# Kernel tuning notes

Hardware: AMD Instinct MI355X
Metric: run time of the kernel (lower is better)

Reference implementation:

```python
import jax, jax.numpy as jnp
import numpy as np
from functools import partial

H = 512
V = 32000


def setup_inputs() -> dict:
    key = jax.random.key(0)
    ks = jax.random.split(key, 16)
    B, Td, Te = 16, 64, 64
    s = 0.02
    inp = {
        'input_seqs': jax.random.normal(ks[0], (B, Td, H), jnp.float32),
        'input_lengths': jax.random.randint(ks[1], (B,), 1, Td + 1, jnp.int32),
        'encoder_outputs': jax.random.normal(ks[2], (B, Te, H), jnp.float32),
        'encoder_length': jax.random.randint(ks[3], (B,), 1, Te + 1, jnp.int32),
        # GRU (1 layer, batch_first): PyTorch layout W_ih (3H,H), W_hh (3H,H)
        'W_ih': jax.random.normal(ks[4], (3 * H, H), jnp.float32) * s,
        'W_hh': jax.random.normal(ks[5], (3 * H, H), jnp.float32) * s,
        'b_ih': jnp.zeros((3 * H,), jnp.float32),
        'b_hh': jnp.zeros((3 * H,), jnp.float32),
        # Attn: W: Linear(2H -> H), v: Linear(H -> 1)
        'W_attn': jax.random.normal(ks[6], (H, 2 * H), jnp.float32) * s,
        'b_attn': jnp.zeros((H,), jnp.float32),
        'v_w': jax.random.normal(ks[7], (H,), jnp.float32) * s,
        'v_b': jnp.zeros((), jnp.float32),
        # dense: Linear(2H -> H), output: Linear(H -> V)
        'W_dense': jax.random.normal(ks[8], (H, 2 * H), jnp.float32) * s,
        'b_dense': jnp.zeros((H,), jnp.float32),
        'W_out': jax.random.normal(ks[9], (V, H), jnp.float32) * s,
        'b_out': jnp.zeros((V,), jnp.float32),
    }
    return inp


def gru_forward(x, lengths, W_ih, W_hh, b_ih, b_hh):
    # Emulates pack_padded_sequence + GRU + pad_packed_sequence:
    # hidden state frozen past each sequence's length, outputs zero there.
    B, T, Hd = x.shape
    x_proj = jnp.einsum('bth,gh->btg', x, W_ih) + b_ih  # (B,T,3H)

    def step(h, inp):
        xp, t = inp  # xp: (B,3H)
        hp = h @ W_hh.T + b_hh
        xr, xz, xn = jnp.split(xp, 3, axis=-1)
        hr, hz, hn = jnp.split(hp, 3, axis=-1)
        r = jax.nn.sigmoid(xr + hr)
        z = jax.nn.sigmoid(xz + hz)
        n = jnp.tanh(xn + r * hn)
        h_new = (1.0 - z) * n + z * h
        valid = (t < lengths)[:, None]
        h_keep = jnp.where(valid, h_new, h)
        y = jnp.where(valid, h_new, 0.0)
        return h_keep, y

    h0 = jnp.zeros((B, Hd), x.dtype)
    h_last, ys = jax.lax.scan(step, h0, (x_proj.swapaxes(0, 1), jnp.arange(T)))
    return ys.swapaxes(0, 1), h_last  # (B,T,H), (B,H)


def attn_forward(enc, dec, enc_len, dec_len, W_attn, b_attn, v_w, v_b):
    B, Te, Hd = enc.shape
    Td = dec.shape[1]
    e_mask = (jnp.arange(Te) < enc_len[:, None])  # (B,Te)
    d_mask = (jnp.arange(Td) < dec_len[:, None])  # (B,Td)
    mask = (d_mask[:, :, None] & e_mask[:, None, :]).astype(enc.dtype)  # (B,Td,Te)
    # split W on the concat axis: cat(enc,dec) @ W.T = enc@We.T + dec@Wd.T
    We, Wd = W_attn[:, :Hd], W_attn[:, Hd:]
    enc_p = jnp.einsum('beh,gh->beg', enc, We)  # (B,Te,H)
    dec_p = jnp.einsum('bdh,gh->bdg', dec, Wd)  # (B,Td,H)
    m4 = mask[..., None]
    # masked-then-projected, matching enc_outputs*mask / dec_outputs*mask in torch
    score = jnp.tanh(enc_p[:, None, :, :] * m4 + dec_p[:, :, None, :] * m4 + b_attn)  # (B,Td,Te,H)
    energy = jnp.einsum('bdeh,h->bde', score, v_w) + v_b  # (B,Td,Te)
    a = jax.nn.softmax(energy, axis=2)  # softmax over ALL Te incl. masked (faithful)
    a_m = a * mask
    s = a_m.sum(axis=2)
    s = jnp.where(s == 0, 1.0, s)
    attention = a_m / s[:, :, None]  # (B,Td,Te)
    # attention is already zero where mask==0, so enc*mask == plain enc here
    context = jnp.einsum('bde,beh->bdh', attention, enc)
    return context  # dropout is identity at eval


def reference(input_seqs, input_lengths, encoder_outputs, encoder_length,
              W_ih, W_hh, b_ih, b_hh, W_attn, b_attn, v_w, v_b,
              W_dense, b_dense, W_out, b_out):
    dec_out, h_last = gru_forward(input_seqs, input_lengths, W_ih, W_hh, b_ih, b_hh)
    context = attn_forward(encoder_outputs, dec_out, encoder_length, input_lengths,
                           W_attn, b_attn, v_w, v_b)
    outputs = jnp.concatenate((dec_out, context), axis=2)  # (B,Td,2H)
    dense = jnp.tanh(jnp.einsum('bdg,hg->bdh', outputs, W_dense) + b_dense)
    logits = jnp.einsum('bdh,vh->bdv', dense, W_out) + b_out  # (B,Td,V)
    return logits, h_last[None]  # hidden: (n_layers=1, B, H)
```

## Files before the change

kernel.cpp:

```cpp
#include <hip/hip_runtime.h>
#include <stdint.h>


#define Hdim 512
#define Vdim 32000
#define Bdim 16
#define Tdim 64
#define BT   1024
#define GANG_BLOCKS 16

typedef __attribute__((ext_vector_type(8))) short bf16x8;
typedef __attribute__((ext_vector_type(4))) float f32x4;

static __device__ __forceinline__ unsigned short f2bf(float f) {
    unsigned u = __float_as_uint(f);
    u = u + 0x7FFFu + ((u >> 16) & 1u);
    return (unsigned short)(u >> 16);
}
static __device__ __forceinline__ float bf2f(unsigned short h) {
    return __uint_as_float((unsigned)h << 16);
}
static __device__ __forceinline__ float fast_tanh(float x) {
    return 2.f / (1.f + __expf(-2.f * x)) - 1.f;
}


#define U_ZERO 8320
#define U_INP  131072
#define U_WIH  196608
#define U_WAT  131072
#define U_WDE  131072
#define U_ENC  131072
#define U_SPLIT (U_INP + U_WIH + U_WAT + U_WDE + U_ENC)
#define U_WOUT 4096000
#define U_TOT  (U_ZERO + U_SPLIT + U_WOUT)

__global__ __launch_bounds__(256) void preproc_kernel(
    const float* __restrict__ input_seqs,
    const float* __restrict__ W_ih,
    const float* __restrict__ W_attn,
    const float* __restrict__ W_dense,
    const float* __restrict__ enc,
    const float* __restrict__ W_out,
    float* __restrict__ zero_base,
    unsigned short* __restrict__ inp_h, unsigned short* __restrict__ inp_l,
    unsigned short* __restrict__ Wih_h, unsigned short* __restrict__ Wih_l,
    unsigned short* __restrict__ Wat_h, unsigned short* __restrict__ Wat_l,
    unsigned short* __restrict__ Wde_h, unsigned short* __restrict__ Wde_l,
    unsigned short* __restrict__ enc_h, unsigned short* __restrict__ enc_l,
    unsigned short* __restrict__ Wout_bf)
{
    int u = blockIdx.x * 256 + threadIdx.x;
    const int stride = gridDim.x * 256;
    for (; u < U_TOT; u += stride) {
        int r = u;
        if (r < U_ZERO) {
            float4 z; z.x = 0.f; z.y = 0.f; z.z = 0.f; z.w = 0.f;
            *(float4*)(zero_base + r * 4) = z;
            continue;
        }
        r -= U_ZERO;
        if (r >= U_SPLIT) {
            int i = (r - U_SPLIT) * 4;
            float4 v = *(const float4*)(W_out + i);
            unsigned short h[4] = {f2bf(v.x), f2bf(v.y), f2bf(v.z), f2bf(v.w)};
            *(uint2*)(Wout_bf + i) = *(const uint2*)h;
            continue;
        }
        const float* src; unsigned short* hi; unsigned short* lo;
        if (r < U_INP) { src = input_seqs; hi = inp_h; lo = inp_l; }
        else { r -= U_INP;
            if (r < U_WIH) { src = W_ih; hi = Wih_h; lo = Wih_l; }
            else { r -= U_WIH;
                if (r < U_WAT) { src = W_attn; hi = Wat_h; lo = Wat_l; }
                else { r -= U_WAT;
                    if (r < U_WDE) { src = W_dense; hi = Wde_h; lo = Wde_l; }
                    else { r -= U_WDE; src = enc; hi = enc_h; lo = enc_l; }
                }
            }
        }
        int i = r * 4;
        float4 v = *(const float4*)(src + i);
        float f[4] = {v.x, v.y, v.z, v.w};
        unsigned short h[4], l[4];
#pragma unroll
        for (int k = 0; k < 4; ++k) {
            h[k] = f2bf(f[k]);
            l[k] = f2bf(f[k] - bf2f(h[k]));
        }
        *(uint2*)(hi + i) = *(const uint2*)h;
        *(uint2*)(lo + i) = *(const uint2*)l;
    }
}


__global__ __launch_bounds__(256) void gemm_split(
    const unsigned short* __restrict__ Ah, const unsigned short* __restrict__ Al, int lda,
    const unsigned short* __restrict__ Bh, const unsigned short* __restrict__ Bl, int ldb,
    const float* __restrict__ bias,
    float* __restrict__ C, unsigned short* __restrict__ Cb, int ldc,
    int K, int act)
{
    __shared__ unsigned short AsH[128 * 40];
    __shared__ unsigned short AsL[128 * 40];
    __shared__ unsigned short BsH[128 * 40];
    __shared__ unsigned short BsL[128 * 40];
    const int tid = threadIdx.x;
    const int m0 = blockIdx.y * 128, n0 = blockIdx.x * 128;
    const int wave = tid >> 6, lane = tid & 63;
    const int wm = (wave >> 1) * 64, wn = (wave & 1) * 64;
    const int lrow = lane & 15, lk = (lane >> 4) * 8;

    f32x4 acc[4][4];
#pragma unroll
    for (int i = 0; i < 4; ++i)
#pragma unroll
        for (int j = 0; j < 4; ++j) acc[i][j] = (f32x4){0.f, 0.f, 0.f, 0.f};

    for (int k0 = 0; k0 < K; k0 += 32) {
#pragma unroll
        for (int i = 0; i < 2; ++i) {
            int idx = tid + i * 256;
            int rr = idx >> 2, kq = (idx & 3) * 8;
            size_t ao = (size_t)(m0 + rr) * lda + k0 + kq;
            size_t bo = (size_t)(n0 + rr) * ldb + k0 + kq;
            *(uint4*)(&AsH[rr * 40 + kq]) = *(const uint4*)(Ah + ao);
            *(uint4*)(&AsL[rr * 40 + kq]) = *(const uint4*)(Al + ao);
            *(uint4*)(&BsH[rr * 40 + kq]) = *(const uint4*)(Bh + bo);
            *(uint4*)(&BsL[rr * 40 + kq]) = *(const uint4*)(Bl + bo);
        }
        __syncthreads();
        bf16x8 ah[4], al[4], bh[4], bl[4];
#pragma unroll
        for (int i = 0; i < 4; ++i) {
            ah[i] = *(const bf16x8*)(&AsH[(wm + i * 16 + lrow) * 40 + lk]);
            al[i] = *(const bf16x8*)(&AsL[(wm + i * 16 + lrow) * 40 + lk]);
        }
#pragma unroll
        for (int j = 0; j < 4; ++j) {
            bh[j] = *(const bf16x8*)(&BsH[(wn + j * 16 + lrow) * 40 + lk]);
            bl[j] = *(const bf16x8*)(&BsL[(wn + j * 16 + lrow) * 40 + lk]);
        }
#pragma unroll
        for (int i = 0; i < 4; ++i)
#pragma unroll
            for (int j = 0; j < 4; ++j) {
                acc[i][j] = __builtin_amdgcn_mfma_f32_16x16x32_bf16(ah[i], bh[j], acc[i][j], 0, 0, 0);
                acc[i][j] = __builtin_amdgcn_mfma_f32_16x16x32_bf16(ah[i], bl[j], acc[i][j], 0, 0, 0);
                acc[i][j] = __builtin_amdgcn_mfma_f32_16x16x32_bf16(al[i], bh[j], acc[i][j], 0, 0, 0);
            }
        __syncthreads();
    }

    const int crow = m0 + wm + ((lane >> 4) * 4);
    const int ccol = n0 + wn + (lane & 15);
#pragma unroll
    for (int i = 0; i < 4; ++i) {
#pragma unroll
        for (int j = 0; j < 4; ++j) {
            int col = ccol + j * 16;
            float bv = bias[col];
#pragma unroll
            for (int rr = 0; rr < 4; ++rr) {
                int row = crow + i * 16 + rr;
                float v = acc[i][j][rr] + bv;
                if (act == 1) v = fast_tanh(v);
                if (Cb) Cb[(size_t)row * ldc + col] = f2bf(v);
                else    C [(size_t)row * ldc + col] = v;
            }
        }
    }
}


__global__ __launch_bounds__(640) void gru_persistent(
    const float* __restrict__ xp,
    const float* __restrict__ Whh,
    const float* __restrict__ bhh,
    const int*   __restrict__ lengths,
    unsigned long long* __restrict__ hslots,
    unsigned short* __restrict__ cath,
    unsigned short* __restrict__ catl,
    float* __restrict__ h_last)
{
    const int bid  = blockIdx.x;
    const int b    = bid >> 4;
    const int blk  = bid & 15;
    const int tid  = threadIdx.x;
    const int wave = tid >> 6, lane = tid & 63;

    __shared__ float hl[2][512];
    __shared__ unsigned short yh_buf[64][32];
    __shared__ unsigned short yl_buf[64][32];

    const size_t PSTR = (size_t)Bdim * Hdim;
    unsigned long long* gslot = hslots + (size_t)b * Hdim;

    if (wave < 2) {
        const int qb = wave * 4;
        for (int t = 0; t < Tdim; ++t) {
            const int par = t & 1;
            const unsigned long long* sl =
                gslot + (size_t)par * PSTR + lane * 8 + qb;
            unsigned long long v[4];
            bool ok;
            do {
#pragma unroll
                for (int q = 0; q < 4; ++q)
                    v[q] = __hip_atomic_load(sl + q, __ATOMIC_RELAXED,
                                             __HIP_MEMORY_SCOPE_AGENT);
                ok = true;
#pragma unroll
                for (int q = 0; q < 4; ++q)
                    ok = ok && ((unsigned)(v[q] >> 32) == (unsigned)t);
            } while (!ok);
#pragma unroll
            for (int q = 0; q < 4; ++q)
                hl[par][(qb + q) * 64 + lane] =
                    __uint_as_float((unsigned)v[q]);
            __syncthreads();
        }
    } else {
        const int cw = wave - 2;
        const int j0 = blk * 32 + cw * 4;
        const int k0 = lane * 8;

        float w[12][8];
#pragma unroll
        for (int g = 0; g < 3; ++g)
#pragma unroll
            for (int jj = 0; jj < 4; ++jj) {
                const float* src = Whh + (size_t)(g * 512 + j0 + jj) * Hdim + k0;
                float4 a = *(const float4*)src;
                float4 bq = *(const float4*)(src + 4);
                int r = g * 4 + jj;
                w[r][0] = a.x;  w[r][1] = a.y;  w[r][2] = a.z;  w[r][3] = a.w;
                w[r][4] = bq.x; w[r][5] = bq.y; w[r][6] = bq.z; w[r][7] = bq.w;
            }

        const int j = j0 + (lane & 3);
        float bh_r = 0.f, bh_z = 0.f, bh_n = 0.f;
        if (lane < 4) {
            bh_r = bhh[j]; bh_z = bhh[512 + j]; bh_n = bhh[1024 + j];
        }
        const int len_b = lengths[b];
        float hprev = 0.f;
        const float* xbase = xp + (size_t)b * Tdim * 1536;

        for (int t = 0; t < Tdim; ++t) {
            const int par = t & 1;

            float xr = 0.f, xz = 0.f, xn = 0.f;
            if (lane < 4) {
                const float* xrow = xbase + (size_t)t * 1536;
                xr = xrow[j]; xz = xrow[512 + j]; xn = xrow[1024 + j];
            }
            __syncthreads();

            float hv[8];
#pragma unroll
            for (int q = 0; q < 8; ++q) hv[q] = hl[par][q * 64 + lane];

            float p[12];
#pragma unroll
            for (int r = 0; r < 12; ++r) {
                float s = 0.f;
#pragma unroll
                for (int k = 0; k < 8; ++k) s += w[r][k] * hv[k];
                p[r] = s;
            }

#pragma unroll
            for (int off = 1; off < 64; off <<= 1)
#pragma unroll
                for (int r = 0; r < 12; ++r)
                    p[r] += __shfl_xor(p[r], off);

            if (lane < 4) {
                const int jj = lane;
                float hr = p[jj]     + bh_r;
                float hz = p[4 + jj] + bh_z;
                float hn = p[8 + jj] + bh_n;
                float rg = 1.f / (1.f + __expf(-(xr + hr)));
                float zg = 1.f / (1.f + __expf(-(xz + hz)));
                float ng = fast_tanh(xn + rg * hn);
                float hnew = (1.f - zg) * ng + zg * hprev;
                bool valid = t < len_b;
                float hkeep = valid ? hnew : hprev;
                hprev = hkeep;
                if (t < Tdim - 1) {
                    unsigned long long pv =
                        ((unsigned long long)(unsigned)(t + 1) << 32) |
                        (unsigned long long)__float_as_uint(hkeep);
                    __hip_atomic_exchange(
                        gslot + (size_t)((t + 1) & 1) * PSTR + j, pv,
                        __ATOMIC_RELAXED, __HIP_MEMORY_SCOPE_AGENT);
                } else {
                    h_last[b * Hdim + j] = hkeep;
                }
                float y = valid ? hnew : 0.f;
                unsigned short yh = f2bf(y);
                yh_buf[t][cw * 4 + jj] = yh;
                yl_buf[t][cw * 4 + jj] = f2bf(y - bf2f(yh));
            }
        }
    }

    __syncthreads();
    for (int idx = tid; idx < 64 * 16; idx += 640) {
        int t = idx >> 4, c = (idx & 15) * 2;
        size_t off = (size_t)(b * Tdim + t) * 1024 + blk * 32 + c;
        *(unsigned*)(cath + off) = *(const unsigned*)(&yh_buf[t][c]);
        *(unsigned*)(catl + off) = *(const unsigned*)(&yl_buf[t][c]);
    }
}


__global__ __launch_bounds__(256) void attn_kernel(
    const float* __restrict__ encp,
    const float* __restrict__ decp,
    const float* __restrict__ enc,
    const float* __restrict__ battn,
    const float* __restrict__ vw,
    const float* __restrict__ vb,
    const int* __restrict__ enc_len,
    const int* __restrict__ dec_len,
    unsigned short* __restrict__ cath,
    unsigned short* __restrict__ catl)
{
    const int blk = blockIdx.x;
    const int b = blk >> 6, d = blk & 63;
    const int tid = threadIdx.x;
    const size_t obase = (size_t)(b * Tdim + d) * 1024 + 512;

    if (d >= dec_len[b]) {
        for (int h = tid; h < Hdim; h += 256) { cath[obase + h] = 0; catl[obase + h] = 0; }
        return;
    }
    const int Tv = enc_len[b];

    __shared__ float part[64][4];
    __shared__ float a_lds[64];

    const int e = tid >> 2, p = tid & 3;
    float s = 0.f;
    if (e < Tv) {
        const float* ep = encp + (size_t)(b * Tdim + e) * Hdim;
        const float* dp = decp + (size_t)(b * Tdim + d) * Hdim;
        const int g0 = p * 128;
        for (int g = g0; g < g0 + 128; ++g)
            s += vw[g] * fast_tanh(ep[g] + dp[g] + battn[g]);
    }
    part[e][p] = s;
    __syncthreads();

    if (tid < 64) {
        const int e2 = tid;
        float en = (e2 < Tv) ? (part[e2][0] + part[e2][1] + part[e2][2] + part[e2][3] + vb[0]) : -1e30f;
        float m = en;
#pragma unroll
        for (int off = 32; off; off >>= 1) m = fmaxf(m, __shfl_xor(m, off));
        float ex = (e2 < Tv) ? __expf(en - m) : 0.f;
        float sum = ex;
#pragma unroll
        for (int off = 32; off; off >>= 1) sum += __shfl_xor(sum, off);
        a_lds[e2] = ex / sum;
    }
    __syncthreads();

    const int h = tid * 2;
    float c0 = 0.f, c1 = 0.f;
    for (int e3 = 0; e3 < Tv; ++e3) {
        float a = a_lds[e3];
        float2 ev = *(const float2*)(enc + (size_t)(b * Tdim + e3) * Hdim + h);
        c0 += a * ev.x; c1 += a * ev.y;
    }
    unsigned short h0 = f2bf(c0), h1 = f2bf(c1);
    cath[obase + h]     = h0;  catl[obase + h]     = f2bf(c0 - bf2f(h0));
    cath[obase + h + 1] = h1;  catl[obase + h + 1] = f2bf(c1 - bf2f(h1));
}


__global__ __launch_bounds__(256) void gemm_logits(
    const unsigned short* __restrict__ A,
    const unsigned short* __restrict__ B,
    const float* __restrict__ bias,
    float* __restrict__ C)
{
    const int K = Hdim;
    __shared__ unsigned short As[128 * 40];
    __shared__ unsigned short Bs[128 * 40];
    const int tid = threadIdx.x;
    const int m0 = blockIdx.y * 128, n0 = blockIdx.x * 128;
    const int wave = tid >> 6, lane = tid & 63;
    const int wm = (wave >> 1) * 64, wn = (wave & 1) * 64;
    const int lrow = lane & 15, lk = (lane >> 4) * 8;

    f32x4 acc[4][4];
#pragma unroll
    for (int i = 0; i < 4; ++i)
#pragma unroll
        for (int j = 0; j < 4; ++j) acc[i][j] = (f32x4){0.f, 0.f, 0.f, 0.f};

    for (int k0 = 0; k0 < K; k0 += 32) {
#pragma unroll
        for (int i = 0; i < 2; ++i) {
            int idx = tid + i * 256;
            int rr = idx >> 2, kq = (idx & 3) * 8;
            *(uint4*)(&As[rr * 40 + kq]) = *(const uint4*)(A + (size_t)(m0 + rr) * K + k0 + kq);
            *(uint4*)(&Bs[rr * 40 + kq]) = *(const uint4*)(B + (size_t)(n0 + rr) * K + k0 + kq);
        }
        __syncthreads();
        bf16x8 af[4], bf[4];
#pragma unroll
        for (int i = 0; i < 4; ++i) af[i] = *(const bf16x8*)(&As[(wm + i * 16 + lrow) * 40 + lk]);
#pragma unroll
        for (int j = 0; j < 4; ++j) bf[j] = *(const bf16x8*)(&Bs[(wn + j * 16 + lrow) * 40 + lk]);
#pragma unroll
        for (int i = 0; i < 4; ++i)
#pragma unroll
            for (int j = 0; j < 4; ++j)
                acc[i][j] = __builtin_amdgcn_mfma_f32_16x16x32_bf16(af[i], bf[j], acc[i][j], 0, 0, 0);
        __syncthreads();
    }

    const int crow = m0 + wm + ((lane >> 4) * 4);
    const int ccol = n0 + wn + (lane & 15);
#pragma unroll
    for (int i = 0; i < 4; ++i) {
#pragma unroll
        for (int j = 0; j < 4; ++j) {
            int col = ccol + j * 16;
            float bv = bias[col];
#pragma unroll
            for (int rr = 0; rr < 4; ++rr) {
                int row = crow + i * 16 + rr;
                C[(size_t)row * Vdim + col] = acc[i][j][rr] + bv;
            }
        }
    }
}


extern "C" void kernel_launch(void* const* d_in, const int* in_sizes, int n_in,
                              void* d_out, int out_size, void* d_ws, size_t ws_size,
                              hipStream_t stream) {
    (void)in_sizes; (void)n_in; (void)out_size; (void)ws_size;

    const float* input_seqs  = (const float*)d_in[0];
    const int*   input_len   = (const int*)  d_in[1];
    const float* enc_out     = (const float*)d_in[2];
    const int*   enc_len     = (const int*)  d_in[3];
    const float* W_ih        = (const float*)d_in[4];
    const float* W_hh        = (const float*)d_in[5];
    const float* b_ih        = (const float*)d_in[6];
    const float* b_hh        = (const float*)d_in[7];
    const float* W_attn      = (const float*)d_in[8];
    const float* b_attn      = (const float*)d_in[9];
    const float* v_w         = (const float*)d_in[10];
    const float* v_b         = (const float*)d_in[11];
    const float* W_dense     = (const float*)d_in[12];
    const float* b_dense     = (const float*)d_in[13];
    const float* W_out       = (const float*)d_in[14];
    const float* b_out       = (const float*)d_in[15];

    float* logits = (float*)d_out;
    float* h_last = (float*)d_out + (size_t)BT * Vdim;

    float* ws    = (float*)d_ws;
    float* xp    = ws;
    float* encp  = xp   + 1572864;
    float* decp  = encp + 524288;
    unsigned long long* hslots = (unsigned long long*)(decp + 524288);
    float* zbias = (float*)(hslots + 16384);
    unsigned short* U0 = (unsigned short*)(zbias + 512);
    unsigned short* inp_h   = U0;
    unsigned short* inp_l   = U0 + 524288;
    unsigned short* Wih_h   = U0 + 1048576;
    unsigned short* Wih_l   = U0 + 1835008;
    unsigned short* Wattn_h = U0 + 2621440;
    unsigned short* Wattn_l = U0 + 3145728;
    unsigned short* Wden_h  = U0 + 3670016;
    unsigned short* Wden_l  = U0 + 4194304;
    unsigned short* enc_h   = U0 + 4718592;
    unsigned short* enc_l   = U0 + 5242880;
    unsigned short* Wout_bf = U0 + 5767168;
    unsigned short* cath = U0;
    unsigned short* catl = U0 + 1048576;
    unsigned short* dense_bf = (unsigned short*)encp;

    preproc_kernel<<<4096, 256, 0, stream>>>(
        input_seqs, W_ih, W_attn, W_dense, enc_out, W_out,
        (float*)hslots,
        inp_h, inp_l, Wih_h, Wih_l, Wattn_h, Wattn_l,
        Wden_h, Wden_l, enc_h, enc_l, Wout_bf);

    gemm_split<<<dim3(1536 / 128, BT / 128), 256, 0, stream>>>(
        inp_h, inp_l, Hdim, Wih_h, Wih_l, Hdim, b_ih, xp, nullptr, 1536, Hdim, 0);

    gemm_split<<<dim3(Hdim / 128, BT / 128), 256, 0, stream>>>(
        enc_h, enc_l, Hdim, Wattn_h, Wattn_l, 1024, zbias, encp, nullptr, Hdim, Hdim, 0);

    gru_persistent<<<Bdim * GANG_BLOCKS, 640, 0, stream>>>(
        xp, W_hh, b_hh, input_len, hslots, cath, catl, h_last);

    gemm_split<<<dim3(Hdim / 128, BT / 128), 256, 0, stream>>>(
        cath, catl, 1024, Wattn_h + 512, Wattn_l + 512, 1024, zbias, decp, nullptr, Hdim, Hdim, 0);

    attn_kernel<<<BT, 256, 0, stream>>>(encp, decp, enc_out, b_attn, v_w, v_b,
                                        enc_len, input_len, cath, catl);

    gemm_split<<<dim3(Hdim / 128, BT / 128), 256, 0, stream>>>(
        cath, catl, 1024, Wden_h, Wden_l, 1024, b_dense, nullptr, dense_bf, Hdim, 1024, 1);

    gemm_logits<<<dim3(Vdim / 128, BT / 128), 256, 0, stream>>>(
        dense_bf, Wout_bf, b_out, logits);
}
```

Measured before the change: 709.3 us.

## Restructure GRU gang to 8 blocks of 1024 threads and merge input GEMMs

The persistent GRU now runs 8 blocks of 16 waves per batch row instead of 16 blocks of 10 waves. The dedicated poller waves are gone: wave 0 polls the hidden-state slots inline, every wave computes, and the slots are padded to a 2-word stride to spread them across cache lines. Atomic exchange becomes a plain atomic store. Separately, the W_ih projection GEMM and the encoder-attention projection GEMM are merged into one dual launch. The aim is fewer participants in each cross-block sync per timestep and one fewer launch, at the cost of losing the overlap between polling and compute.

Result: slower. 1.138 ms (+60.5%).

```diff
diff --git a/kernel.cpp b/kernel.cpp
--- a/kernel.cpp
+++ b/kernel.cpp
@@ -7,7 +7,7 @@
 #define Bdim 16
 #define Tdim 64
 #define BT   1024
-#define GANG_BLOCKS 16
+#define GANG_BLOCKS 8
 
 typedef __attribute__((ext_vector_type(8))) short bf16x8;
 typedef __attribute__((ext_vector_type(4))) float f32x4;
@@ -25,7 +25,7 @@
 }
 
 
-#define U_ZERO 8320
+#define U_ZERO 16512
 #define U_INP  131072
 #define U_WIH  196608
 #define U_WAT  131072
@@ -94,19 +94,22 @@
 }
 
 
-__global__ __launch_bounds__(256) void gemm_split(
+struct GemmSmem {
+    unsigned short AsH[128 * 40];
+    unsigned short AsL[128 * 40];
+    unsigned short BsH[128 * 40];
+    unsigned short BsL[128 * 40];
+};
+
+static __device__ __forceinline__ void gemm_tile(
+    GemmSmem& S, int m0, int n0,
     const unsigned short* __restrict__ Ah, const unsigned short* __restrict__ Al, int lda,
     const unsigned short* __restrict__ Bh, const unsigned short* __restrict__ Bl, int ldb,
     const float* __restrict__ bias,
     float* __restrict__ C, unsigned short* __restrict__ Cb, int ldc,
     int K, int act)
 {
-    __shared__ unsigned short AsH[128 * 40];
-    __shared__ unsigned short AsL[128 * 40];
-    __shared__ unsigned short BsH[128 * 40];
-    __shared__ unsigned short BsL[128 * 40];
     const int tid = threadIdx.x;
-    const int m0 = blockIdx.y * 128, n0 = blockIdx.x * 128;
     const int wave = tid >> 6, lane = tid & 63;
     const int wm = (wave >> 1) * 64, wn = (wave & 1) * 64;
     const int lrow = lane & 15, lk = (lane >> 4) * 8;
@@ -124,22 +127,22 @@
             int rr = idx >> 2, kq = (idx & 3) * 8;
             size_t ao = (size_t)(m0 + rr) * lda + k0 + kq;
             size_t bo = (size_t)(n0 + rr) * ldb + k0 + kq;
-            *(uint4*)(&AsH[rr * 40 + kq]) = *(const uint4*)(Ah + ao);
-            *(uint4*)(&AsL[rr * 40 + kq]) = *(const uint4*)(Al + ao);
-            *(uint4*)(&BsH[rr * 40 + kq]) = *(const uint4*)(Bh + bo);
-            *(uint4*)(&BsL[rr * 40 + kq]) = *(const uint4*)(Bl + bo);
+            *(uint4*)(&S.AsH[rr * 40 + kq]) = *(const uint4*)(Ah + ao);
+            *(uint4*)(&S.AsL[rr * 40 + kq]) = *(const uint4*)(Al + ao);
+            *(uint4*)(&S.BsH[rr * 40 + kq]) = *(const uint4*)(Bh + bo);
+            *(uint4*)(&S.BsL[rr * 40 + kq]) = *(const uint4*)(Bl + bo);
         }
         __syncthreads();
         bf16x8 ah[4], al[4], bh[4], bl[4];
 #pragma unroll
         for (int i = 0; i < 4; ++i) {
-            ah[i] = *(const bf16x8*)(&AsH[(wm + i * 16 + lrow) * 40 + lk]);
-            al[i] = *(const bf16x8*)(&AsL[(wm + i * 16 + lrow) * 40 + lk]);
+            ah[i] = *(const bf16x8*)(&S.AsH[(wm + i * 16 + lrow) * 40 + lk]);
+            al[i] = *(const bf16x8*)(&S.AsL[(wm + i * 16 + lrow) * 40 + lk]);
         }
 #pragma unroll
         for (int j = 0; j < 4; ++j) {
-            bh[j] = *(const bf16x8*)(&BsH[(wn + j * 16 + lrow) * 40 + lk]);
-            bl[j] = *(const bf16x8*)(&BsL[(wn + j * 16 + lrow) * 40 + lk]);
+            bh[j] = *(const bf16x8*)(&S.BsH[(wn + j * 16 + lrow) * 40 + lk]);
+            bl[j] = *(const bf16x8*)(&S.BsL[(wn + j * 16 + lrow) * 40 + lk]);
         }
 #pragma unroll
         for (int i = 0; i < 4; ++i)
@@ -172,8 +175,40 @@
     }
 }
 
-
-__global__ __launch_bounds__(640) void gru_persistent(
+__global__ __launch_bounds__(256) void gemm_split(
+    const unsigned short* __restrict__ Ah, const unsigned short* __restrict__ Al, int lda,
+    const unsigned short* __restrict__ Bh, const unsigned short* __restrict__ Bl, int ldb,
+    const float* __restrict__ bias,
+    float* __restrict__ C, unsigned short* __restrict__ Cb, int ldc,
+    int K, int act)
+{
+    __shared__ GemmSmem S;
+    gemm_tile(S, blockIdx.y * 128, blockIdx.x * 128,
+              Ah, Al, lda, Bh, Bl, ldb, bias, C, Cb, ldc, K, act);
+}
+
+__global__ __launch_bounds__(256) void gemm_split_dual(
+    const unsigned short* __restrict__ A0h, const unsigned short* __restrict__ A0l,
+    const unsigned short* __restrict__ B0h, const unsigned short* __restrict__ B0l,
+    const float* __restrict__ bias0, float* __restrict__ C0,
+    const unsigned short* __restrict__ A1h, const unsigned short* __restrict__ A1l,
+    const unsigned short* __restrict__ B1h, const unsigned short* __restrict__ B1l,
+    const float* __restrict__ bias1, float* __restrict__ C1)
+{
+    __shared__ GemmSmem S;
+    const int bid = blockIdx.x;
+    if (bid < 96) {
+        gemm_tile(S, (bid / 12) * 128, (bid % 12) * 128,
+                  A0h, A0l, Hdim, B0h, B0l, Hdim, bias0, C0, nullptr, 1536, Hdim, 0);
+    } else {
+        int r = bid - 96;
+        gemm_tile(S, (r / 4) * 128, (r % 4) * 128,
+                  A1h, A1l, Hdim, B1h, B1l, 1024, bias1, C1, nullptr, Hdim, Hdim, 0);
+    }
+}
+
+
+__global__ __launch_bounds__(1024) void gru_persistent(
     const float* __restrict__ xp,
     const float* __restrict__ Whh,
     const float* __restrict__ bhh,
@@ -184,132 +219,123 @@
     float* __restrict__ h_last)
 {
     const int bid  = blockIdx.x;
-    const int b    = bid >> 4;
-    const int blk  = bid & 15;
+    const int b    = bid >> 3;
+    const int blk  = bid & 7;
     const int tid  = threadIdx.x;
     const int wave = tid >> 6, lane = tid & 63;
+    const int j0 = blk * 64 + wave * 4;
+    const int k0 = lane * 8;
 
     __shared__ float hl[2][512];
-    __shared__ unsigned short yh_buf[64][32];
-    __shared__ unsigned short yl_buf[64][32];
-
-    const size_t PSTR = (size_t)Bdim * Hdim;
-    unsigned long long* gslot = hslots + (size_t)b * Hdim;
-
-    if (wave < 2) {
-        const int qb = wave * 4;
-        for (int t = 0; t < Tdim; ++t) {
-            const int par = t & 1;
+    __shared__ unsigned short yh_buf[64][64];
+    __shared__ unsigned short yl_buf[64][64];
+
+    unsigned long long* gslot = hslots + (size_t)b * 2048;
+
+    float w[12][8];
+#pragma unroll
+    for (int g = 0; g < 3; ++g)
+#pragma unroll
+        for (int jj = 0; jj < 4; ++jj) {
+            const float* src = Whh + (size_t)(g * 512 + j0 + jj) * Hdim + k0;
+            float4 a = *(const float4*)src;
+            float4 bq = *(const float4*)(src + 4);
+            int r = g * 4 + jj;
+            w[r][0] = a.x;  w[r][1] = a.y;  w[r][2] = a.z;  w[r][3] = a.w;
+            w[r][4] = bq.x; w[r][5] = bq.y; w[r][6] = bq.z; w[r][7] = bq.w;
+        }
+
+    const int j = j0 + (lane & 3);
+    float bh_r = 0.f, bh_z = 0.f, bh_n = 0.f;
+    if (lane < 4) {
+        bh_r = bhh[j]; bh_z = bhh[512 + j]; bh_n = bhh[1024 + j];
+    }
+    const int len_b = lengths[b];
+    float hprev = 0.f;
+    const float* xbase = xp + (size_t)b * Tdim * 1536;
+
+    for (int t = 0; t < Tdim; ++t) {
+        const int par = t & 1;
+
+        float xr = 0.f, xz = 0.f, xn = 0.f;
+        if (lane < 4) {
+            const float* xrow = xbase + (size_t)t * 1536;
+            xr = xrow[j]; xz = xrow[512 + j]; xn = xrow[1024 + j];
+        }
+
+        if (wave == 0) {
             const unsigned long long* sl =
-                gslot + (size_t)par * PSTR + lane * 8 + qb;
-            unsigned long long v[4];
+                gslot + (size_t)par * 1024 + (size_t)lane * 16;
+            unsigned long long v[8];
             bool ok;
             do {
 #pragma unroll
-                for (int q = 0; q < 4; ++q)
-                    v[q] = __hip_atomic_load(sl + q, __ATOMIC_RELAXED,
+                for (int q = 0; q < 8; ++q)
+                    v[q] = __hip_atomic_load(sl + q * 2, __ATOMIC_RELAXED,
                                              __HIP_MEMORY_SCOPE_AGENT);
                 ok = true;
 #pragma unroll
-                for (int q = 0; q < 4; ++q)
+                for (int q = 0; q < 8; ++q)
                     ok = ok && ((unsigned)(v[q] >> 32) == (unsigned)t);
             } while (!ok);
 #pragma unroll
-            for (int q = 0; q < 4; ++q)
-                hl[par][(qb + q) * 64 + lane] =
-                    __uint_as_float((unsigned)v[q]);
-            __syncthreads();
-        }
-    } else {
-        const int cw = wave - 2;
-        const int j0 = blk * 32 + cw * 4;
-        const int k0 = lane * 8;
-
-        float w[12][8];
-#pragma unroll
-        for (int g = 0; g < 3; ++g)
-#pragma unroll
-            for (int jj = 0; jj < 4; ++jj) {
-                const float* src = Whh + (size_t)(g * 512 + j0 + jj) * Hdim + k0;
-                float4 a = *(const float4*)src;
-                float4 bq = *(const float4*)(src + 4);
-                int r = g * 4 + jj;
-                w[r][0] = a.x;  w[r][1] = a.y;  w[r][2] = a.z;  w[r][3] = a.w;
-                w[r][4] = bq.x; w[r][5] = bq.y; w[r][6] = bq.z; w[r][7] = bq.w;
+            for (int q = 0; q < 8; ++q)
+                hl[par][q * 64 + lane] = __uint_as_float((unsigned)v[q]);
+        }
+        __syncthreads();
+
+        float hv[8];
+#pragma unroll
+        for (int q = 0; q < 8; ++q) hv[q] = hl[par][q * 64 + lane];
+
+        float p[12];
+#pragma unroll
+        for (int r = 0; r < 12; ++r) {
+            float s = 0.f;
+#pragma unroll
+            for (int k = 0; k < 8; ++k) s += w[r][k] * hv[k];
+            p[r] = s;
+        }
+
+#pragma unroll
+        for (int off = 1; off < 64; off <<= 1)
+#pragma unroll
+            for (int r = 0; r < 12; ++r)
+                p[r] += __shfl_xor(p[r], off);
+
+        if (lane < 4) {
+            const int jj = lane;
+            float hr = p[jj]     + bh_r;
+            float hz = p[4 + jj] + bh_z;
+            float hn = p[8 + jj] + bh_n;
+            float rg = 1.f / (1.f + __expf(-(xr + hr)));
+            float zg = 1.f / (1.f + __expf(-(xz + hz)));
+            float ng = fast_tanh(xn + rg * hn);
+            float hnew = (1.f - zg) * ng + zg * hprev;
+            bool valid = t < len_b;
+            float hkeep = valid ? hnew : hprev;
+            hprev = hkeep;
+            if (t < Tdim - 1) {
+                unsigned long long pv =
+                    ((unsigned long long)(unsigned)(t + 1) << 32) |
+                    (unsigned long long)__float_as_uint(hkeep);
+                __hip_atomic_store(
+                    gslot + (size_t)((t + 1) & 1) * 1024 + (size_t)j * 2, pv,
+                    __ATOMIC_RELAXED, __HIP_MEMORY_SCOPE_AGENT);
+            } else {
+                h_last[b * Hdim + j] = hkeep;
             }
-
-        const int j = j0 + (lane & 3);
-        float bh_r = 0.f, bh_z = 0.f, bh_n = 0.f;
-        if (lane < 4) {
-            bh_r = bhh[j]; bh_z = bhh[512 + j]; bh_n = bhh[1024 + j];
-        }
-        const int len_b = lengths[b];
-        float hprev = 0.f;
-        const float* xbase = xp + (size_t)b * Tdim * 1536;
-
-        for (int t = 0; t < Tdim; ++t) {
-            const int par = t & 1;
-
-            float xr = 0.f, xz = 0.f, xn = 0.f;
-            if (lane < 4) {
-                const float* xrow = xbase + (size_t)t * 1536;
-                xr = xrow[j]; xz = xrow[512 + j]; xn = xrow[1024 + j];
-            }
-            __syncthreads();
-
-            float hv[8];
-#pragma unroll
-            for (int q = 0; q < 8; ++q) hv[q] = hl[par][q * 64 + lane];
-
-            float p[12];
-#pragma unroll
-            for (int r = 0; r < 12; ++r) {
-                float s = 0.f;
-#pragma unroll
-                for (int k = 0; k < 8; ++k) s += w[r][k] * hv[k];
-                p[r] = s;
-            }
-
-#pragma unroll
-            for (int off = 1; off < 64; off <<= 1)
-#pragma unroll
-                for (int r = 0; r < 12; ++r)
-                    p[r] += __shfl_xor(p[r], off);
-
-            if (lane < 4) {
-                const int jj = lane;
-                float hr = p[jj]     + bh_r;
-                float hz = p[4 + jj] + bh_z;
-                float hn = p[8 + jj] + bh_n;
-                float rg = 1.f / (1.f + __expf(-(xr + hr)));
-                float zg = 1.f / (1.f + __expf(-(xz + hz)));
-                float ng = fast_tanh(xn + rg * hn);
-                float hnew = (1.f - zg) * ng + zg * hprev;
-                bool valid = t < len_b;
-                float hkeep = valid ? hnew : hprev;
-                hprev = hkeep;
-                if (t < Tdim - 1) {
-                    unsigned long long pv =
-                        ((unsigned long long)(unsigned)(t + 1) << 32) |
-                        (unsigned long long)__float_as_uint(hkeep);
-                    __hip_atomic_exchange(
-                        gslot + (size_t)((t + 1) & 1) * PSTR + j, pv,
-                        __ATOMIC_RELAXED, __HIP_MEMORY_SCOPE_AGENT);
-                } else {
-                    h_last[b * Hdim + j] = hkeep;
-                }
-                float y = valid ? hnew : 0.f;
-                unsigned short yh = f2bf(y);
-                yh_buf[t][cw * 4 + jj] = yh;
-                yl_buf[t][cw * 4 + jj] = f2bf(y - bf2f(yh));
-            }
+            float y = valid ? hnew : 0.f;
+            unsigned short yh = f2bf(y);
+            yh_buf[t][wave * 4 + jj] = yh;
+            yl_buf[t][wave * 4 + jj] = f2bf(y - bf2f(yh));
         }
     }
 
     __syncthreads();
-    for (int idx = tid; idx < 64 * 16; idx += 640) {
-        int t = idx >> 4, c = (idx & 15) * 2;
-        size_t off = (size_t)(b * Tdim + t) * 1024 + blk * 32 + c;
+    for (int idx = tid; idx < 64 * 32; idx += 1024) {
+        int t = idx >> 5, c = (idx & 31) * 2;
+        size_t off = (size_t)(b * Tdim + t) * 1024 + blk * 64 + c;
         *(unsigned*)(cath + off) = *(const unsigned*)(&yh_buf[t][c]);
         *(unsigned*)(catl + off) = *(const unsigned*)(&yl_buf[t][c]);
     }
@@ -472,7 +498,7 @@
     float* encp  = xp   + 1572864;
     float* decp  = encp + 524288;
     unsigned long long* hslots = (unsigned long long*)(decp + 524288);
-    float* zbias = (float*)(hslots + 16384);
+    float* zbias = (float*)(hslots + 32768);
     unsigned short* U0 = (unsigned short*)(zbias + 512);
     unsigned short* inp_h   = U0;
     unsigned short* inp_l   = U0 + 524288;
@@ -495,13 +521,11 @@
         inp_h, inp_l, Wih_h, Wih_l, Wattn_h, Wattn_l,
         Wden_h, Wden_l, enc_h, enc_l, Wout_bf);
 
-    gemm_split<<<dim3(1536 / 128, BT / 128), 256, 0, stream>>>(
-        inp_h, inp_l, Hdim, Wih_h, Wih_l, Hdim, b_ih, xp, nullptr, 1536, Hdim, 0);
-
-    gemm_split<<<dim3(Hdim / 128, BT / 128), 256, 0, stream>>>(
-        enc_h, enc_l, Hdim, Wattn_h, Wattn_l, 1024, zbias, encp, nullptr, Hdim, Hdim, 0);
-
-    gru_persistent<<<Bdim * GANG_BLOCKS, 640, 0, stream>>>(
+    gemm_split_dual<<<128, 256, 0, stream>>>(
+        inp_h, inp_l, Wih_h, Wih_l, b_ih, xp,
+        enc_h, enc_l, Wattn_h, Wattn_l, zbias, encp);
+
+    gru_persistent<<<Bdim * GANG_BLOCKS, 1024, 0, stream>>>(
         xp, W_hh, b_hh, input_len, hslots, cath, catl, h_last);
 
     gemm_split<<<dim3(Hdim / 128, BT / 128), 256, 0, stream>>>(
```
